# Optimization experiments

Measured on AMD Instinct MI355X. Metric: run time of the kernel, lower is better.

The kernel has to match this reference:

```python
import jax, jax.numpy as jnp
import numpy as np

TOP_K = 2
SCALING = 16.0 / 8.0  # alpha / rank


def setup_inputs() -> dict:
    key = jax.random.key(0)
    ks = jax.random.split(key, 9)
    B, V, D, P = 32, 21, 512, 64
    IN, OUT, E, R, H = D * P, 96, 8, 8, 256
    return {
        "x": jax.random.normal(ks[0], (B, V, D, P), jnp.float32),
        "W_base": jax.random.normal(ks[1], (OUT, IN), jnp.float32) * (IN ** -0.5),
        "b_base": jax.random.normal(ks[2], (OUT,), jnp.float32) * 0.01,
        "W1": jax.random.normal(ks[3], (H, D), jnp.float32) * (D ** -0.5),
        "b1": jax.random.normal(ks[4], (H,), jnp.float32) * 0.01,
        "W2": jax.random.normal(ks[5], (E, H), jnp.float32) * (H ** -0.5),
        "b2": jax.random.normal(ks[6], (E,), jnp.float32) * 0.01,
        "lora_A": jax.random.normal(ks[7], (E, R, IN), jnp.float32) * (IN ** -0.5),
        "lora_B": jax.random.normal(ks[8], (E, OUT, R), jnp.float32) * (R ** -0.5),
    }


def reference(x, W_base, b_base, W1, b1, W2, b2, lora_A, lora_B):
    B, V, D, P = x.shape
    E = lora_A.shape[0]
    # FlattenHead: flatten last two dims, then linear (dropout is identity in eval)
    flat = x.reshape(B, V, D * P)                      # [B, V, IN]
    base_out = flat @ W_base.T + b_base                # [B, V, OUT]
    # Router: pool over n_vars then patch dim -> [B, D]
    pooled = x.mean(axis=1).mean(axis=-1)
    h = jax.nn.relu(pooled @ W1.T + b1)
    logits = h @ W2.T + b2                             # [B, E]
    probs = jax.nn.softmax(logits, axis=-1)
    topw, topi = jax.lax.top_k(probs, TOP_K)           # [B, K]
    topw = topw / jnp.clip(topw.sum(-1, keepdims=True), 1e-6)
    # All LoRA experts (matches original dense compute), then weighted combine
    temp = jnp.einsum("bvi,eri->ebvr", flat, lora_A)   # [E, B, V, R]
    delta = jnp.einsum("ebvr,eor->ebvo", temp, lora_B) * SCALING  # [E, B, V, OUT]
    # Scatter top-k weights into dense [B, E] then combine (top-k sparse combine)
    w_full = jnp.zeros((B, E), x.dtype).at[jnp.arange(B)[:, None], topi].add(topw)
    moe_delta = jnp.einsum("be,ebvo->bvo", w_full, delta)
    return base_out + moe_delta, probs
```

## Files before the change

kernel.cpp:

```cpp
#include <hip/hip_runtime.h>

#define B_DIM 32
#define V_DIM 21
#define D_DIM 512
#define P_DIM 64
#define M_TOTAL 672
#define K_TOTAL 32768
#define OUT_DIM 96
#define E_DIM 8
#define R_DIM 8
#define H_DIM 256
#define N_TOTAL 160
#define SCALING 2.0f
#define POOL_SCALE (1.0f / (V_DIM * (float)P_DIM))

#define BM 96
#define BK 32
#define KSPLIT 32
#define K_PER_SPLIT (K_TOTAL / KSPLIT)
#define CHUNKS (K_PER_SPLIT / BK)
#define SMN (M_TOTAL * N_TOTAL)
#define NMB 7
#define RC_ROWS 4

typedef __attribute__((ext_vector_type(4))) float floatx4;
typedef __attribute__((ext_vector_type(8))) short short8;

__device__ __forceinline__ unsigned short f2bf(float f) {
  union { float f; unsigned int u; } v; v.f = f;
  unsigned int u = v.u + (0x7FFFu + ((v.u >> 16) & 1u));
  return (unsigned short)(u >> 16);
}

__device__ __forceinline__ unsigned int cvt_pk_bf16(float lo, float hi) {
  unsigned int r;
  asm("v_cvt_pk_bf16_f32 %0, %1, %2" : "=v"(r) : "v"(lo), "v"(hi));
  return r;
}

__global__ __launch_bounds__(256)
void convW_kernel(const float* __restrict__ W_base, const float* __restrict__ lora_A,
                  short* __restrict__ Wb) {
  int gid = blockIdx.x * 256 + threadIdx.x;
  size_t base = (size_t)gid * 8;
  int row = (int)(base >> 15);
  int k = (int)(base & 32767);
  const float* src = (row < OUT_DIM) ? (W_base + ((size_t)row << 15) + k)
                                     : (lora_A + ((size_t)(row - OUT_DIM) << 15) + k);
  floatx4 v0 = ((const floatx4*)src)[0];
  floatx4 v1 = ((const floatx4*)src)[1];
  short8 sv;
  sv[0] = (short)f2bf(v0[0]); sv[1] = (short)f2bf(v0[1]);
  sv[2] = (short)f2bf(v0[2]); sv[3] = (short)f2bf(v0[3]);
  sv[4] = (short)f2bf(v1[0]); sv[5] = (short)f2bf(v1[1]);
  sv[6] = (short)f2bf(v1[2]); sv[7] = (short)f2bf(v1[3]);
  int ky = k >> 10, c = (k >> 5) & 31, quad = (k >> 3) & 3;
  int nt = row >> 4, l16 = row & 15;
  size_t off = ((size_t)(ky * 32 + c) * 10 + nt) * 512 + l16 * 32 + quad * 8;
  *(short8*)(Wb + off) = sv;
}

__global__ __launch_bounds__(384)
void gemm_kernel(const float* __restrict__ x, const short* __restrict__ Wb,
                 float* __restrict__ P, float* __restrict__ pp) {
  __shared__ float lds_pool[6 * 16];

  const int tid = threadIdx.x;
  const int bid = blockIdx.x;
  const int xcd = bid & 7;
  const int grp = bid >> 3;
  const int ky  = xcd + 8 * (grp / NMB);
  const int mb  = grp % NMB;
  const int m0 = mb * BM;
  const int kbase = ky * K_PER_SPLIT;
  const int lane = tid & 63;
  const int wave = tid >> 6;
  const int quad = lane >> 4;
  const int l16 = lane & 15;
  const int b_first = m0 / V_DIM;

  if (tid < 96) lds_pool[tid] = 0.0f;
  asm volatile("s_waitcnt lgkmcnt(0)" ::: "memory");
  __builtin_amdgcn_s_barrier();

  const int arow = m0 + wave * 16 + l16;
  const floatx4* aptr =
      (const floatx4*)(x + (size_t)arow * K_TOTAL + kbase + quad * 8);
  const short* bbase = Wb + (size_t)ky * (CHUNKS * 5120) + l16 * 32 + quad * 8;
  const int pool_idx = (arow / V_DIM - b_first) * 16;

  short8 bf[2][10];
  floatx4 af[4][2];
  floatx4 acc[10];
  #pragma unroll
  for (int nt = 0; nt < 10; ++nt) acc[nt] = (floatx4)(0.0f);
  floatx4 paccv = (floatx4)(0.0f);

  #pragma unroll
  for (int nt = 0; nt < 10; ++nt)
    bf[0][nt] = *(const short8*)(bbase + nt * 512);
  #pragma unroll
  for (int nt = 0; nt < 10; ++nt)
    bf[1][nt] = *(const short8*)(bbase + 5120 + nt * 512);
  af[0][0] = aptr[0];  af[0][1] = aptr[1];
  af[1][0] = aptr[8];  af[1][1] = aptr[9];
  af[2][0] = aptr[16]; af[2][1] = aptr[17];
  af[3][0] = aptr[24]; af[3][1] = aptr[25];

  #pragma unroll
  for (int c = 0; c < CHUNKS; ++c) {
    const int ab = c & 3, bb = c & 1;
    floatx4 f0 = af[ab][0], f1 = af[ab][1];
    if (c + 4 < CHUNKS) {
      af[ab][0] = aptr[(c + 4) * 8];
      af[ab][1] = aptr[(c + 4) * 8 + 1];
    }
    union { short8 s; unsigned int u[4]; } av;
    av.u[0] = cvt_pk_bf16(f0[0], f0[1]);
    av.u[1] = cvt_pk_bf16(f0[2], f0[3]);
    av.u[2] = cvt_pk_bf16(f1[0], f1[1]);
    av.u[3] = cvt_pk_bf16(f1[2], f1[3]);
    paccv += f0 + f1;
    if (c & 1) {
      float h = (paccv[0] + paccv[1]) + (paccv[2] + paccv[3]);
      h += __shfl_down(h, 32);
      h += __shfl_down(h, 16);
      if (lane < 16)
        atomicAdd(&lds_pool[pool_idx + (c >> 1)], h);
      paccv = (floatx4)(0.0f);
    }
    #pragma unroll
    for (int nt = 0; nt < 10; ++nt)
      acc[nt] = __builtin_amdgcn_mfma_f32_16x16x32_bf16(av.s, bf[bb][nt],
                                                        acc[nt], 0, 0, 0);
    if (c + 2 < CHUNKS) {
      #pragma unroll
      for (int nt = 0; nt < 10; ++nt)
        bf[bb][nt] = *(const short8*)(bbase + (c + 2) * 5120 + nt * 512);
    }
  }

  __syncthreads();

  {
    const int mrow = m0 + wave * 16 + quad * 4;
    float* Pp = P + (size_t)ky * SMN + (size_t)mrow * N_TOTAL + l16;
    #pragma unroll
    for (int r = 0; r < 4; ++r)
      #pragma unroll
      for (int nt = 0; nt < 10; ++nt)
        Pp[(size_t)r * N_TOTAL + nt * 16] = acc[nt][r];
  }

  if (tid < 96) {
    int bl = tid >> 4, dl = tid & 15;
    pp[((size_t)(mb * 6 + bl)) * D_DIM + ky * 16 + dl] = lds_pool[tid];
  }
}

__global__ __launch_bounds__(256)
void router_kernel(const float* __restrict__ pp, const float* __restrict__ W1,
                   const float* __restrict__ b1, const float* __restrict__ W2,
                   const float* __restrict__ b2, float* __restrict__ wfull,
                   float* __restrict__ probs_out) {
  __shared__ float sp[D_DIM];
  __shared__ float sh[H_DIM];
  __shared__ float slog[E_DIM];
  const int b = blockIdx.x;
  const int t = threadIdx.x;
  const int mb1 = (b * V_DIM) / BM;
  const int mb2 = (b * V_DIM + V_DIM - 1) / BM;
  const int bf1 = (mb1 * BM) / V_DIM;
  const int bf2 = (mb2 * BM) / V_DIM;
  const float* p1 = pp + (size_t)(mb1 * 6 + (b - bf1)) * D_DIM;
  const float* p2 = pp + (size_t)(mb2 * 6 + (b - bf2)) * D_DIM;
  for (int d = t; d < D_DIM; d += 256) {
    float v = p1[d];
    if (mb2 != mb1) v += p2[d];
    sp[d] = v * POOL_SCALE;
  }
  __syncthreads();
  float acc = b1[t];
  const float* w1r = W1 + (size_t)t * D_DIM;
  for (int d = 0; d < D_DIM; ++d) acc += sp[d] * w1r[d];
  sh[t] = fmaxf(acc, 0.0f);
  __syncthreads();
  if (t < E_DIM) {
    float a = b2[t];
    const float* w2r = W2 + t * H_DIM;
    for (int j = 0; j < H_DIM; ++j) a += sh[j] * w2r[j];
    slog[t] = a;
  }
  __syncthreads();
  if (t == 0) {
    float p[E_DIM];
    float mx = slog[0];
    for (int e = 1; e < E_DIM; ++e) mx = fmaxf(mx, slog[e]);
    float se = 0.0f;
    for (int e = 0; e < E_DIM; ++e) { p[e] = __expf(slog[e] - mx); se += p[e]; }
    float inv = 1.0f / se;
    for (int e = 0; e < E_DIM; ++e) { p[e] *= inv; probs_out[b * E_DIM + e] = p[e]; }
    int i0 = 0;
    for (int e = 1; e < E_DIM; ++e) if (p[e] > p[i0]) i0 = e;
    int i1 = (i0 == 0) ? 1 : 0;
    for (int e = 0; e < E_DIM; ++e) if (e != i0 && p[e] > p[i1]) i1 = e;
    float s2 = p[i0] + p[i1];
    float invs = 1.0f / fmaxf(s2, 1e-6f);
    for (int e = 0; e < E_DIM; ++e) {
      float w = 0.0f;
      if (e == i0) w += p[i0] * invs;
      if (e == i1) w += p[i1] * invs;
      wfull[b * E_DIM + e] = w;
    }
  }
}

__global__ __launch_bounds__(256)
void reduce_combine_kernel(const float* __restrict__ P, const float* __restrict__ b_base,
                           const float* __restrict__ lora_B, const float* __restrict__ wfull,
                           float* __restrict__ out) {
  __shared__ float sS[RC_ROWS * N_TOTAL];
  const int t = threadIdx.x;
  const int NF4 = RC_ROWS * N_TOTAL / 4;
  if (t < NF4) {
    const floatx4* P4 = (const floatx4*)P;
    size_t base = (size_t)blockIdx.x * NF4 + t;
    floatx4 a = (floatx4)(0.0f);
    #pragma unroll 8
    for (int k = 0; k < KSPLIT; ++k) a += P4[(size_t)k * (SMN / 4) + base];
    *(floatx4*)&sS[t * 4] = a;
  }
  __syncthreads();
  for (int i = t; i < RC_ROWS * OUT_DIM; i += 256) {
    int mr = i / OUT_DIM;
    int o = i - mr * OUT_DIM;
    int mm = blockIdx.x * RC_ROWS + mr;
    int b = mm / V_DIM;
    const float* srow = sS + mr * N_TOTAL;
    float res = srow[o] + b_base[o];
    float moe = 0.0f;
    #pragma unroll
    for (int e = 0; e < E_DIM; ++e) {
      float we = wfull[b * E_DIM + e];
      if (we != 0.0f) {
        const float* lb = lora_B + ((size_t)e * OUT_DIM + o) * R_DIM;
        float dd = 0.0f;
        #pragma unroll
        for (int r = 0; r < R_DIM; ++r) dd += srow[OUT_DIM + e * R_DIM + r] * lb[r];
        moe += we * dd;
      }
    }
    out[(size_t)mm * OUT_DIM + o] = res + SCALING * moe;
  }
}

extern "C" void kernel_launch(void* const* d_in, const int* in_sizes, int n_in,
                              void* d_out, int out_size, void* d_ws, size_t ws_size,
                              hipStream_t stream) {
  const float* x      = (const float*)d_in[0];
  const float* W_base = (const float*)d_in[1];
  const float* b_base = (const float*)d_in[2];
  const float* W1     = (const float*)d_in[3];
  const float* b1     = (const float*)d_in[4];
  const float* W2     = (const float*)d_in[5];
  const float* b2     = (const float*)d_in[6];
  const float* lora_A = (const float*)d_in[7];
  const float* lora_B = (const float*)d_in[8];
  float* out = (float*)d_out;

  float* ws    = (float*)d_ws;
  float* pp    = ws;
  float* wfull = ws + NMB * 6 * D_DIM;
  short* Wb    = (short*)(wfull + 256);
  float* P     = (float*)(Wb + (size_t)N_TOTAL * K_TOTAL);

  convW_kernel<<<(N_TOTAL * K_TOTAL / 8 + 255) / 256, 256, 0, stream>>>(
      W_base, lora_A, Wb);
  gemm_kernel<<<NMB * KSPLIT, 384, 0, stream>>>(x, Wb, P, pp);
  router_kernel<<<B_DIM, 256, 0, stream>>>(pp, W1, b1, W2, b2, wfull,
                                           out + (size_t)M_TOTAL * OUT_DIM);
  reduce_combine_kernel<<<M_TOTAL / RC_ROWS, 256, 0, stream>>>(
      P, b_base, lora_B, wfull, out);
}
```

Before: 219.7 us.

## Retile split-K GEMM to 64-row blocks with 64-way K split and inline B loads

Shrinks the M tile from 96 to 64 rows (4 waves, 11 row blocks with bounds guards) and doubles the K split to 64, which roughly triples the block count for better CU occupancy. It also drops the double-buffered B register prefetch in favour of loading B fragments per step, and requests 3 blocks per CU via launch bounds. The aim is more parallelism and lower register pressure. The cost is extra partial-sum traffic in P, which doubles in size, and more reduction work in the combine kernel; B load latency is now less hidden.

```diff
diff --git a/kernel.cpp b/kernel.cpp
--- a/kernel.cpp
+++ b/kernel.cpp
@@ -14,14 +14,14 @@
 #define SCALING 2.0f
 #define POOL_SCALE (1.0f / (V_DIM * (float)P_DIM))
 
-#define BM 96
+#define BM 64
 #define BK 32
-#define KSPLIT 32
+#define KSPLIT 64
 #define K_PER_SPLIT (K_TOTAL / KSPLIT)
 #define CHUNKS (K_PER_SPLIT / BK)
 #define SMN (M_TOTAL * N_TOTAL)
-#define NMB 7
-#define RC_ROWS 4
+#define NMB 11
+#define RC_ROWS 6
 
 typedef __attribute__((ext_vector_type(4))) float floatx4;
 typedef __attribute__((ext_vector_type(8))) short short8;
@@ -54,16 +54,16 @@
   sv[2] = (short)f2bf(v0[2]); sv[3] = (short)f2bf(v0[3]);
   sv[4] = (short)f2bf(v1[0]); sv[5] = (short)f2bf(v1[1]);
   sv[6] = (short)f2bf(v1[2]); sv[7] = (short)f2bf(v1[3]);
-  int ky = k >> 10, c = (k >> 5) & 31, quad = (k >> 3) & 3;
+  int ky = k >> 9, c = (k >> 5) & 15, quad = (k >> 3) & 3;
   int nt = row >> 4, l16 = row & 15;
-  size_t off = ((size_t)(ky * 32 + c) * 10 + nt) * 512 + l16 * 32 + quad * 8;
+  size_t off = ((size_t)(ky * 16 + c) * 10 + nt) * 512 + l16 * 32 + quad * 8;
   *(short8*)(Wb + off) = sv;
 }
 
-__global__ __launch_bounds__(384)
+__global__ __launch_bounds__(256, 3)
 void gemm_kernel(const float* __restrict__ x, const short* __restrict__ Wb,
                  float* __restrict__ P, float* __restrict__ pp) {
-  __shared__ float lds_pool[6 * 16];
+  __shared__ float lds_pool[5 * 8];
 
   const int tid = threadIdx.x;
   const int bid = blockIdx.x;
@@ -79,82 +79,85 @@
   const int l16 = lane & 15;
   const int b_first = m0 / V_DIM;
 
-  if (tid < 96) lds_pool[tid] = 0.0f;
-  asm volatile("s_waitcnt lgkmcnt(0)" ::: "memory");
-  __builtin_amdgcn_s_barrier();
-
-  const int arow = m0 + wave * 16 + l16;
+  if (tid < 40) lds_pool[tid] = 0.0f;
+  __syncthreads();
+
+  const int arow_raw = m0 + wave * 16 + l16;
+  const bool row_ok = (arow_raw < M_TOTAL);
+  const int arow = row_ok ? arow_raw : (M_TOTAL - 1);
   const floatx4* aptr =
       (const floatx4*)(x + (size_t)arow * K_TOTAL + kbase + quad * 8);
   const short* bbase = Wb + (size_t)ky * (CHUNKS * 5120) + l16 * 32 + quad * 8;
-  const int pool_idx = (arow / V_DIM - b_first) * 16;
-
-  short8 bf[2][10];
-  floatx4 af[4][2];
-  floatx4 acc[10];
-  #pragma unroll
-  for (int nt = 0; nt < 10; ++nt) acc[nt] = (floatx4)(0.0f);
+  const int pool_idx = (arow / V_DIM - b_first) * 8;
+
+  floatx4 acc0 = (floatx4)(0.0f), acc1 = (floatx4)(0.0f), acc2 = (floatx4)(0.0f),
+          acc3 = (floatx4)(0.0f), acc4 = (floatx4)(0.0f), acc5 = (floatx4)(0.0f),
+          acc6 = (floatx4)(0.0f), acc7 = (floatx4)(0.0f), acc8 = (floatx4)(0.0f),
+          acc9 = (floatx4)(0.0f);
   floatx4 paccv = (floatx4)(0.0f);
 
-  #pragma unroll
-  for (int nt = 0; nt < 10; ++nt)
-    bf[0][nt] = *(const short8*)(bbase + nt * 512);
-  #pragma unroll
-  for (int nt = 0; nt < 10; ++nt)
-    bf[1][nt] = *(const short8*)(bbase + 5120 + nt * 512);
-  af[0][0] = aptr[0];  af[0][1] = aptr[1];
-  af[1][0] = aptr[8];  af[1][1] = aptr[9];
-  af[2][0] = aptr[16]; af[2][1] = aptr[17];
-  af[3][0] = aptr[24]; af[3][1] = aptr[25];
-
-  #pragma unroll
-  for (int c = 0; c < CHUNKS; ++c) {
-    const int ab = c & 3, bb = c & 1;
-    floatx4 f0 = af[ab][0], f1 = af[ab][1];
-    if (c + 4 < CHUNKS) {
-      af[ab][0] = aptr[(c + 4) * 8];
-      af[ab][1] = aptr[(c + 4) * 8 + 1];
-    }
-    union { short8 s; unsigned int u[4]; } av;
-    av.u[0] = cvt_pk_bf16(f0[0], f0[1]);
-    av.u[1] = cvt_pk_bf16(f0[2], f0[3]);
-    av.u[2] = cvt_pk_bf16(f1[0], f1[1]);
-    av.u[3] = cvt_pk_bf16(f1[2], f1[3]);
-    paccv += f0 + f1;
-    if (c & 1) {
-      float h = (paccv[0] + paccv[1]) + (paccv[2] + paccv[3]);
-      h += __shfl_down(h, 32);
-      h += __shfl_down(h, 16);
-      if (lane < 16)
-        atomicAdd(&lds_pool[pool_idx + (c >> 1)], h);
-      paccv = (floatx4)(0.0f);
-    }
-    #pragma unroll
-    for (int nt = 0; nt < 10; ++nt)
-      acc[nt] = __builtin_amdgcn_mfma_f32_16x16x32_bf16(av.s, bf[bb][nt],
-                                                        acc[nt], 0, 0, 0);
-    if (c + 2 < CHUNKS) {
-      #pragma unroll
-      for (int nt = 0; nt < 10; ++nt)
-        bf[bb][nt] = *(const short8*)(bbase + (c + 2) * 5120 + nt * 512);
-    }
-  }
+  floatx4 af00 = aptr[0],  af01 = aptr[1];
+  floatx4 af10 = aptr[8],  af11 = aptr[9];
+  floatx4 af20 = aptr[16], af21 = aptr[17];
+  floatx4 af30 = aptr[24], af31 = aptr[25];
+
+#define MFMA(d, a, b) d = __builtin_amdgcn_mfma_f32_16x16x32_bf16(a, b, d, 0, 0, 0)
+
+#define GSTEP(c, AB)                                                          \
+  {                                                                           \
+    const short8* bc = (const short8*)(bbase + (c) * 5120);                   \
+    short8 b0 = bc[0],   b1 = bc[64],  b2 = bc[128], b3 = bc[192],            \
+           b4 = bc[256], b5 = bc[320], b6 = bc[384], b7 = bc[448],            \
+           b8 = bc[512], b9 = bc[576];                                        \
+    floatx4 f0 = af##AB##0, f1 = af##AB##1;                                   \
+    if ((c) + 4 < CHUNKS) {                                                   \
+      af##AB##0 = aptr[((c) + 4) * 8];                                        \
+      af##AB##1 = aptr[((c) + 4) * 8 + 1];                                    \
+    }                                                                         \
+    union { short8 s; unsigned int u[4]; } av;                                \
+    av.u[0] = cvt_pk_bf16(f0[0], f0[1]);                                      \
+    av.u[1] = cvt_pk_bf16(f0[2], f0[3]);                                      \
+    av.u[2] = cvt_pk_bf16(f1[0], f1[1]);                                      \
+    av.u[3] = cvt_pk_bf16(f1[2], f1[3]);                                      \
+    paccv += f0 + f1;                                                         \
+    if ((c) & 1) {                \
+      float h = (paccv[0] + paccv[1]) + (paccv[2] + paccv[3]);                \
+      h += __shfl_down(h, 32);                                                \
+      h += __shfl_down(h, 16);                                                \
+      if (lane < 16 && row_ok)                                                \
+        atomicAdd(&lds_pool[pool_idx + ((c) >> 1)], h);                       \
+      paccv = (floatx4)(0.0f);                                                \
+    }                                                                         \
+    MFMA(acc0, av.s, b0); MFMA(acc1, av.s, b1); MFMA(acc2, av.s, b2);         \
+    MFMA(acc3, av.s, b3); MFMA(acc4, av.s, b4); MFMA(acc5, av.s, b5);         \
+    MFMA(acc6, av.s, b6); MFMA(acc7, av.s, b7); MFMA(acc8, av.s, b8);         \
+    MFMA(acc9, av.s, b9);                                                     \
+  }
+
+  GSTEP(0, 0)  GSTEP(1, 1)  GSTEP(2, 2)  GSTEP(3, 3)
+  GSTEP(4, 0)  GSTEP(5, 1)  GSTEP(6, 2)  GSTEP(7, 3)
+  GSTEP(8, 0)  GSTEP(9, 1)  GSTEP(10, 2) GSTEP(11, 3)
+  GSTEP(12, 0) GSTEP(13, 1) GSTEP(14, 2) GSTEP(15, 3)
+#undef GSTEP
+#undef MFMA
 
   __syncthreads();
 
   {
     const int mrow = m0 + wave * 16 + quad * 4;
     float* Pp = P + (size_t)ky * SMN + (size_t)mrow * N_TOTAL + l16;
+    floatx4 accs[10] = {acc0, acc1, acc2, acc3, acc4, acc5, acc6, acc7, acc8, acc9};
     #pragma unroll
     for (int r = 0; r < 4; ++r)
-      #pragma unroll
-      for (int nt = 0; nt < 10; ++nt)
-        Pp[(size_t)r * N_TOTAL + nt * 16] = acc[nt][r];
-  }
-
-  if (tid < 96) {
-    int bl = tid >> 4, dl = tid & 15;
-    pp[((size_t)(mb * 6 + bl)) * D_DIM + ky * 16 + dl] = lds_pool[tid];
+      if (mrow + r < M_TOTAL)
+        #pragma unroll
+        for (int nt = 0; nt < 10; ++nt)
+          Pp[(size_t)r * N_TOTAL + nt * 16] = accs[nt][r];
+  }
+
+  if (tid < 40) {
+    int bl = tid >> 3, dl = tid & 7;
+    pp[((size_t)(mb * 5 + bl)) * D_DIM + ky * 8 + dl] = lds_pool[tid];
   }
 }
 
@@ -172,8 +175,8 @@
   const int mb2 = (b * V_DIM + V_DIM - 1) / BM;
   const int bf1 = (mb1 * BM) / V_DIM;
   const int bf2 = (mb2 * BM) / V_DIM;
-  const float* p1 = pp + (size_t)(mb1 * 6 + (b - bf1)) * D_DIM;
-  const float* p2 = pp + (size_t)(mb2 * 6 + (b - bf2)) * D_DIM;
+  const float* p1 = pp + (size_t)(mb1 * 5 + (b - bf1)) * D_DIM;
+  const float* p2 = pp + (size_t)(mb2 * 5 + (b - bf2)) * D_DIM;
   for (int d = t; d < D_DIM; d += 256) {
     float v = p1[d];
     if (mb2 != mb1) v += p2[d];
@@ -270,13 +273,13 @@
 
   float* ws    = (float*)d_ws;
   float* pp    = ws;
-  float* wfull = ws + NMB * 6 * D_DIM;
+  float* wfull = ws + NMB * 5 * D_DIM;
   short* Wb    = (short*)(wfull + 256);
   float* P     = (float*)(Wb + (size_t)N_TOTAL * K_TOTAL);
 
   convW_kernel<<<(N_TOTAL * K_TOTAL / 8 + 255) / 256, 256, 0, stream>>>(
       W_base, lora_A, Wb);
-  gemm_kernel<<<NMB * KSPLIT, 384, 0, stream>>>(x, Wb, P, pp);
+  gemm_kernel<<<NMB * KSPLIT, 256, 0, stream>>>(x, Wb, P, pp);
   router_kernel<<<B_DIM, 256, 0, stream>>>(pp, W1, b1, W2, b2, wfull,
                                            out + (size_t)M_TOTAL * OUT_DIM);
   reduce_combine_kernel<<<M_TOTAL / RC_ROWS, 256, 0, stream>>>(
```

Result: no change. 222.9 us (+1.5%).
